# Kernel optimization log

Measured on AMD Instinct MI355X. Metric: run time of the kernel, lower is better.

## Reference

```python
import jax, jax.numpy as jnp
import numpy as np

B, N, F_IN, F_OUT = 8, 8192, 128, 128
EPS = 1e-12  # F.normalize default eps


def setup_inputs() -> dict:
    key = jax.random.key(0)
    k1, k2, k3, k4 = jax.random.split(key, 4)
    x = jax.random.normal(k1, (B, N, F_IN), dtype=jnp.float32)
    adj = jax.random.uniform(k2, (N, N), dtype=jnp.float32)
    weight = jax.random.normal(k3, (F_IN, F_OUT), dtype=jnp.float32) * 0.05
    bias = jax.random.normal(k4, (F_OUT,), dtype=jnp.float32) * 0.05
    return {"x": x, "adj": adj, "weight": weight, "bias": bias}


def reference(x, adj, weight, bias):
    # Aggregate: equivalent to torch.sparse.mm(adj, x^T.reshape(N, B*F)) then
    # un-reshape/transpose — i.e. y[b] = adj @ x[b] for every batch element.
    y = jnp.einsum('nm,bmf->bnf', adj, x)  # [B, N, F_in]
    y = y + x                               # add_self
    y = jnp.einsum('bnf,fo->bno', y, weight) + bias  # dense transform + bias
    # L2 normalize along feature dim (F.normalize, p=2, dim=2)
    norm = jnp.sqrt(jnp.sum(y * y, axis=2, keepdims=True))
    y = y / jnp.maximum(norm, EPS)
    return y
```

## Files before the change

### kernel.cpp

```cpp
#include <hip/hip_runtime.h>
#include <hip/hip_bf16.h>
#include <stdint.h>


typedef __bf16 bf16;
typedef __bf16 bf16x4 __attribute__((ext_vector_type(4)));
typedef __bf16 bf16x8 __attribute__((ext_vector_type(8)));
typedef float floatx4 __attribute__((ext_vector_type(4)));

#define B_ 8
#define N_ 8192
#define F_ 128

__device__ __forceinline__ void async_copy16(const void* g, void* l) {
  __builtin_amdgcn_global_load_lds(
      (const __attribute__((address_space(1))) uint32_t*)g,
      (__attribute__((address_space(3))) uint32_t*)l, 16, 0, 0);
}

__global__ __launch_bounds__(256, 2) void k0_xw_t(const float* __restrict__ x,
                                                  const float* __restrict__ w,
                                                  bf16* __restrict__ ut) {
  __shared__ bf16 As[128][128];
  __shared__ bf16 Wt[128][128];
  const int tid = threadIdx.x;
  const int lane = tid & 63;
  const int l15 = lane & 15;
  const int h = lane >> 4;
  const int wv = tid >> 6;
  const int wr = wv >> 1;
  const int wc = wv & 1;
  const int bm0 = blockIdx.x << 7;
  const int b = bm0 >> 13;
  const int m0 = bm0 & (N_ - 1);

#pragma unroll
  for (int c = 0; c < 64; ++c) {
    int lin = (c << 8) + tid;
    int f = lin >> 7, o = lin & 127;
    bf16 v = (bf16)w[(size_t)f * F_ + o];
    int phys = (f >> 3) ^ (o & 15);
    ((bf16*)Wt)[o * 128 + (phys << 3) + (f & 7)] = v;
  }

  {
    const int r = tid >> 1;
    const int colh = (tid & 1) << 6;
    const float* xr = x + (size_t)(bm0 + r) * F_ + colh;
#pragma unroll
    for (int q = 0; q < 8; ++q) {
      float4 f0 = *(const float4*)(xr + 8 * q);
      float4 f1 = *(const float4*)(xr + 8 * q + 4);
      bf16x8 pk;
      pk[0] = (bf16)f0.x; pk[1] = (bf16)f0.y; pk[2] = (bf16)f0.z; pk[3] = (bf16)f0.w;
      pk[4] = (bf16)f1.x; pk[5] = (bf16)f1.y; pk[6] = (bf16)f1.z; pk[7] = (bf16)f1.w;
      int c = ((tid & 1) << 3) + q;
      int phys = c ^ (r & 15);
      *(bf16x8*)&((bf16*)As)[r * 128 + (phys << 3)] = pk;
    }
  }
  __syncthreads();

  const bf16* pa[4][4];
  const bf16* pb[4][4];
#pragma unroll
  for (int i = 0; i < 4; ++i)
#pragma unroll
    for (int kk = 0; kk < 4; ++kk)
      pa[i][kk] = &As[64 * wr + 16 * i + l15][(((kk << 2) + h) ^ l15) << 3];
#pragma unroll
  for (int j = 0; j < 4; ++j)
#pragma unroll
    for (int kk = 0; kk < 4; ++kk)
      pb[j][kk] = &Wt[64 * wc + 16 * j + l15][(((kk << 2) + h) ^ l15) << 3];

  floatx4 acc[4][4] = {};
#pragma unroll
  for (int kk = 0; kk < 4; ++kk) {
    bf16x8 av[4], bv[4];
#pragma unroll
    for (int i = 0; i < 4; ++i) av[i] = *(const bf16x8*)pa[i][kk];
#pragma unroll
    for (int j = 0; j < 4; ++j) bv[j] = *(const bf16x8*)pb[j][kk];
#pragma unroll
    for (int i = 0; i < 4; ++i)
#pragma unroll
      for (int j = 0; j < 4; ++j)
        acc[i][j] = __builtin_amdgcn_mfma_f32_16x16x32_bf16(av[i], bv[j],
                                                            acc[i][j], 0, 0, 0);
  }

  bf16* utb = ut + (size_t)b * F_ * N_;
#pragma unroll
  for (int i = 0; i < 4; ++i)
#pragma unroll
    for (int j = 0; j < 4; ++j) {
      const int o = 64 * wc + 16 * j + l15;
      const int mrow = m0 + 64 * wr + 16 * i + (h << 2);
      bf16x4 pk;
#pragma unroll
      for (int r = 0; r < 4; ++r) pk[r] = (bf16)acc[i][j][r];
      *(bf16x4*)(utb + (size_t)o * N_ + mrow) = pk;
    }
}

__global__ __launch_bounds__(512, 4) void k1_graphconv(const float* __restrict__ adj,
                                                       const bf16* __restrict__ ut,
                                                       const float* __restrict__ bias,
                                                       float* __restrict__ out) {
  __shared__ bf16 As[128][64];
  __shared__ bf16 Bs[128][64];
  __shared__ float ss[2][128];
  const int tid = threadIdx.x;
  const int lane = tid & 63;
  const int wv = tid >> 6;
  const int wr = wv >> 1;
  const int wc = wv & 1;
  const int n0 = blockIdx.x << 7;
  const int b = blockIdx.y;
  const bf16* ub = ut + (size_t)b * F_ * N_;

  const int brow = tid >> 3;
  const int blc = (tid & 7) ^ (brow & 7);
  const bf16* gb0 = ub + (size_t)brow * N_ + (blc << 3);
  const bf16* gb1 = ub + (size_t)(brow + 64) * N_ + (blc << 3);
  bf16* lb0 = (bf16*)Bs + tid * 8;
  bf16* lb1 = (bf16*)Bs + (tid + 512) * 8;

  const int ar = tid >> 2;
  const int kc = (tid & 3) << 4;
  const float* gAb = adj + (size_t)(n0 + ar) * N_ + kc;
  const int pc0 = ((tid & 3) << 1) ^ (ar & 7);
  bf16* lA0 = (bf16*)As + ar * 64 + (pc0 << 3);
  bf16* lA1 = (bf16*)As + ar * 64 + ((pc0 ^ 1) << 3);

  const bf16* pa[2][2];
  const bf16* pb[4][2];
#pragma unroll
  for (int i = 0; i < 2; ++i)
#pragma unroll
    for (int kk = 0; kk < 2; ++kk)
      pa[i][kk] = &As[32 * wr + 16 * i + (lane & 15)]
                     [(((kk << 2) + (lane >> 4)) ^ (lane & 7)) << 3];
#pragma unroll
  for (int j = 0; j < 4; ++j)
#pragma unroll
    for (int kk = 0; kk < 2; ++kk)
      pb[j][kk] = &Bs[64 * wc + 16 * j + (lane & 15)]
                     [(((kk << 2) + (lane >> 4)) ^ (lane & 7)) << 3];

  floatx4 acc[2][4] = {};

  float4 pf[4];
#pragma unroll
  for (int q = 0; q < 4; ++q) pf[q] = *(const float4*)(gAb + 4 * q);

  for (int ks = 0; ks < 128; ++ks) {
    __syncthreads();
    async_copy16(gb0, lb0);
    async_copy16(gb1, lb1);
    gb0 += 64; gb1 += 64;
    bf16x8 lo, hi;
#pragma unroll
    for (int q = 0; q < 2; ++q) {
      float4 f = pf[q];
      lo[4 * q + 0] = (bf16)f.x; lo[4 * q + 1] = (bf16)f.y;
      lo[4 * q + 2] = (bf16)f.z; lo[4 * q + 3] = (bf16)f.w;
    }
#pragma unroll
    for (int q = 0; q < 2; ++q) {
      float4 f = pf[q + 2];
      hi[4 * q + 0] = (bf16)f.x; hi[4 * q + 1] = (bf16)f.y;
      hi[4 * q + 2] = (bf16)f.z; hi[4 * q + 3] = (bf16)f.w;
    }
    *(bf16x8*)lA0 = lo;
    *(bf16x8*)lA1 = hi;
    __syncthreads();
    const float* gn = gAb + ((size_t)((ks + 1) & 127) << 6);
#pragma unroll
    for (int q = 0; q < 4; ++q) pf[q] = *(const float4*)(gn + 4 * q);

#pragma unroll
    for (int kk = 0; kk < 2; ++kk) {
      bf16x8 av[2], bv[4];
#pragma unroll
      for (int i = 0; i < 2; ++i) av[i] = *(const bf16x8*)pa[i][kk];
#pragma unroll
      for (int j = 0; j < 4; ++j) bv[j] = *(const bf16x8*)pb[j][kk];
#pragma unroll
      for (int i = 0; i < 2; ++i)
#pragma unroll
        for (int j = 0; j < 4; ++j)
          acc[i][j] = __builtin_amdgcn_mfma_f32_16x16x32_bf16(av[i], bv[j],
                                                              acc[i][j], 0, 0, 0);
    }
  }

  float bo[4];
#pragma unroll
  for (int j = 0; j < 4; ++j) bo[j] = bias[64 * wc + 16 * j + (lane & 15)];

  float s[2][4];
#pragma unroll
  for (int i = 0; i < 2; ++i)
#pragma unroll
    for (int r = 0; r < 4; ++r) s[i][r] = 0.0f;
#pragma unroll
  for (int i = 0; i < 2; ++i)
#pragma unroll
    for (int j = 0; j < 4; ++j) {
      floatx4 t = acc[i][j];
      const int col = 64 * wc + 16 * j + (lane & 15);
#pragma unroll
      for (int r = 0; r < 4; ++r) {
        const int rowloc = 32 * wr + 16 * i + ((lane >> 4) << 2) + r;
        t[r] += bo[j] + (float)ub[(size_t)col * N_ + n0 + rowloc];
        s[i][r] += t[r] * t[r];
      }
      acc[i][j] = t;
    }
#pragma unroll
  for (int m = 1; m < 16; m <<= 1)
#pragma unroll
    for (int i = 0; i < 2; ++i)
#pragma unroll
      for (int r = 0; r < 4; ++r) s[i][r] += __shfl_xor(s[i][r], m, 16);

  if ((lane & 15) == 0) {
#pragma unroll
    for (int i = 0; i < 2; ++i)
#pragma unroll
      for (int r = 0; r < 4; ++r)
        ss[wc][32 * wr + 16 * i + ((lane >> 4) << 2) + r] = s[i][r];
  }
  __syncthreads();

  const size_t outbase = ((size_t)b * N_ + n0) * F_;
#pragma unroll
  for (int i = 0; i < 2; ++i)
#pragma unroll
    for (int r = 0; r < 4; ++r) {
      int rowloc = 32 * wr + 16 * i + ((lane >> 4) << 2) + r;
      float tot = ss[0][rowloc] + ss[1][rowloc];
      float inv = 1.0f / fmaxf(sqrtf(tot), 1e-12f);
      size_t ro = outbase + (size_t)rowloc * F_ + 64 * wc + (lane & 15);
#pragma unroll
      for (int j = 0; j < 4; ++j)
        out[ro + 16 * j] = acc[i][j][r] * inv;
    }
}

extern "C" void kernel_launch(void* const* d_in, const int* in_sizes, int n_in,
                              void* d_out, int out_size, void* d_ws, size_t ws_size,
                              hipStream_t stream) {
  (void)in_sizes; (void)n_in; (void)out_size; (void)ws_size;
  const float* x    = (const float*)d_in[0];
  const float* adj  = (const float*)d_in[1];
  const float* w    = (const float*)d_in[2];
  const float* bias = (const float*)d_in[3];
  float* out = (float*)d_out;
  bf16* ut = (bf16*)d_ws;

  k0_xw_t<<<dim3(512), dim3(256), 0, stream>>>(x, w, ut);
  k1_graphconv<<<dim3(64, 8), dim3(512), 0, stream>>>(adj, ut, bias, out);
}
```

Measured before the change: 543.3 us.

## Pretranspose weight once and restructure XW kernel to reuse graphconv pipeline

Adds a single-block kernel that converts the weight to bf16 and transposes it once, so each of the 512 XW blocks no longer converts and scatters the full 128x128 fp32 weight with scalar LDS stores. The XW kernel now uses 512 threads, smaller LDS tiles and the same async global-to-LDS K-loop as the main graphconv kernel, which raises occupancy. The cost is an extra kernel launch and a serial dependency. The XW stage is small next to the N×N adjacency GEMM, so the overall effect should be limited.

```diff
diff --git a/kernel.cpp b/kernel.cpp
--- a/kernel.cpp
+++ b/kernel.cpp
@@ -18,15 +18,41 @@
       (__attribute__((address_space(3))) uint32_t*)l, 16, 0, 0);
 }
 
-__global__ __launch_bounds__(256, 2) void k0_xw_t(const float* __restrict__ x,
-                                                  const float* __restrict__ w,
+__global__ __launch_bounds__(256) void k0w(const float* __restrict__ w,
+                                           bf16* __restrict__ wt) {
+  __shared__ bf16 T[128][129];
+  const int tid = threadIdx.x;
+#pragma unroll
+  for (int c = 0; c < 16; ++c) {
+    int lin = (c << 8) + tid;
+    int f = lin >> 5;
+    int g = lin & 31;
+    float4 v = *(const float4*)(w + (size_t)f * F_ + (g << 2));
+    T[f][(g << 2) + 0] = (bf16)v.x;
+    T[f][(g << 2) + 1] = (bf16)v.y;
+    T[f][(g << 2) + 2] = (bf16)v.z;
+    T[f][(g << 2) + 3] = (bf16)v.w;
+  }
+  __syncthreads();
+#pragma unroll
+  for (int c = 0; c < 16; ++c) {
+    int lin = (c << 8) + tid;
+    int o = lin >> 5;
+    int g = lin & 31;
+    bf16x4 pk;
+#pragma unroll
+    for (int q = 0; q < 4; ++q) pk[q] = T[(g << 2) + q][o];
+    *(bf16x4*)(wt + (size_t)o * F_ + (g << 2)) = pk;
+  }
+}
+
+__global__ __launch_bounds__(512, 4) void k0_xw_t(const float* __restrict__ x,
+                                                  const bf16* __restrict__ wt,
                                                   bf16* __restrict__ ut) {
-  __shared__ bf16 As[128][128];
-  __shared__ bf16 Wt[128][128];
+  __shared__ bf16 As[128][64];
+  __shared__ bf16 Bs[128][64];
   const int tid = threadIdx.x;
   const int lane = tid & 63;
-  const int l15 = lane & 15;
-  const int h = lane >> 4;
   const int wv = tid >> 6;
   const int wr = wv >> 1;
   const int wc = wv & 1;
@@ -34,69 +60,90 @@
   const int b = bm0 >> 13;
   const int m0 = bm0 & (N_ - 1);
 
-#pragma unroll
-  for (int c = 0; c < 64; ++c) {
-    int lin = (c << 8) + tid;
-    int f = lin >> 7, o = lin & 127;
-    bf16 v = (bf16)w[(size_t)f * F_ + o];
-    int phys = (f >> 3) ^ (o & 15);
-    ((bf16*)Wt)[o * 128 + (phys << 3) + (f & 7)] = v;
-  }
-
-  {
-    const int r = tid >> 1;
-    const int colh = (tid & 1) << 6;
-    const float* xr = x + (size_t)(bm0 + r) * F_ + colh;
-#pragma unroll
-    for (int q = 0; q < 8; ++q) {
-      float4 f0 = *(const float4*)(xr + 8 * q);
-      float4 f1 = *(const float4*)(xr + 8 * q + 4);
-      bf16x8 pk;
-      pk[0] = (bf16)f0.x; pk[1] = (bf16)f0.y; pk[2] = (bf16)f0.z; pk[3] = (bf16)f0.w;
-      pk[4] = (bf16)f1.x; pk[5] = (bf16)f1.y; pk[6] = (bf16)f1.z; pk[7] = (bf16)f1.w;
-      int c = ((tid & 1) << 3) + q;
-      int phys = c ^ (r & 15);
-      *(bf16x8*)&((bf16*)As)[r * 128 + (phys << 3)] = pk;
-    }
-  }
-  __syncthreads();
-
-  const bf16* pa[4][4];
-  const bf16* pb[4][4];
-#pragma unroll
-  for (int i = 0; i < 4; ++i)
-#pragma unroll
-    for (int kk = 0; kk < 4; ++kk)
-      pa[i][kk] = &As[64 * wr + 16 * i + l15][(((kk << 2) + h) ^ l15) << 3];
+  const int brow = tid >> 3;
+  const int blc = (tid & 7) ^ (brow & 7);
+  const bf16* gb0 = wt + (size_t)brow * F_ + (blc << 3);
+  const bf16* gb1 = wt + (size_t)(brow + 64) * F_ + (blc << 3);
+  bf16* lb0 = (bf16*)Bs + tid * 8;
+  bf16* lb1 = (bf16*)Bs + (tid + 512) * 8;
+
+  const int ar = tid >> 2;
+  const int kc = (tid & 3) << 4;
+  const float* gAb = x + (size_t)(bm0 + ar) * F_ + kc;
+  const int pc0 = ((tid & 3) << 1) ^ (ar & 7);
+  bf16* lA0 = (bf16*)As + ar * 64 + (pc0 << 3);
+  bf16* lA1 = (bf16*)As + ar * 64 + ((pc0 ^ 1) << 3);
+
+  const bf16* pa[2][2];
+  const bf16* pb[4][2];
+#pragma unroll
+  for (int i = 0; i < 2; ++i)
+#pragma unroll
+    for (int kk = 0; kk < 2; ++kk)
+      pa[i][kk] = &As[32 * wr + 16 * i + (lane & 15)]
+                     [(((kk << 2) + (lane >> 4)) ^ (lane & 7)) << 3];
 #pragma unroll
   for (int j = 0; j < 4; ++j)
 #pragma unroll
-    for (int kk = 0; kk < 4; ++kk)
-      pb[j][kk] = &Wt[64 * wc + 16 * j + l15][(((kk << 2) + h) ^ l15) << 3];
-
-  floatx4 acc[4][4] = {};
-#pragma unroll
-  for (int kk = 0; kk < 4; ++kk) {
-    bf16x8 av[4], bv[4];
-#pragma unroll
-    for (int i = 0; i < 4; ++i) av[i] = *(const bf16x8*)pa[i][kk];
-#pragma unroll
-    for (int j = 0; j < 4; ++j) bv[j] = *(const bf16x8*)pb[j][kk];
-#pragma unroll
-    for (int i = 0; i < 4; ++i)
-#pragma unroll
-      for (int j = 0; j < 4; ++j)
-        acc[i][j] = __builtin_amdgcn_mfma_f32_16x16x32_bf16(av[i], bv[j],
-                                                            acc[i][j], 0, 0, 0);
+    for (int kk = 0; kk < 2; ++kk)
+      pb[j][kk] = &Bs[64 * wc + 16 * j + (lane & 15)]
+                     [(((kk << 2) + (lane >> 4)) ^ (lane & 7)) << 3];
+
+  floatx4 acc[2][4] = {};
+
+  float4 pf[4];
+#pragma unroll
+  for (int q = 0; q < 4; ++q) pf[q] = *(const float4*)(gAb + 4 * q);
+
+#pragma unroll
+  for (int ks = 0; ks < 2; ++ks) {
+    __syncthreads();
+    async_copy16(gb0, lb0);
+    async_copy16(gb1, lb1);
+    gb0 += 64; gb1 += 64;
+    bf16x8 lo, hi;
+#pragma unroll
+    for (int q = 0; q < 2; ++q) {
+      float4 f = pf[q];
+      lo[4 * q + 0] = (bf16)f.x; lo[4 * q + 1] = (bf16)f.y;
+      lo[4 * q + 2] = (bf16)f.z; lo[4 * q + 3] = (bf16)f.w;
+    }
+#pragma unroll
+    for (int q = 0; q < 2; ++q) {
+      float4 f = pf[q + 2];
+      hi[4 * q + 0] = (bf16)f.x; hi[4 * q + 1] = (bf16)f.y;
+      hi[4 * q + 2] = (bf16)f.z; hi[4 * q + 3] = (bf16)f.w;
+    }
+    *(bf16x8*)lA0 = lo;
+    *(bf16x8*)lA1 = hi;
+    __syncthreads();
+    const float* gn = gAb + (((ks + 1) & 1) << 6);
+#pragma unroll
+    for (int q = 0; q < 4; ++q) pf[q] = *(const float4*)(gn + 4 * q);
+
+#pragma unroll
+    for (int kk = 0; kk < 2; ++kk) {
+      bf16x8 av[2], bv[4];
+#pragma unroll
+      for (int i = 0; i < 2; ++i) av[i] = *(const bf16x8*)pa[i][kk];
+#pragma unroll
+      for (int j = 0; j < 4; ++j) bv[j] = *(const bf16x8*)pb[j][kk];
+#pragma unroll
+      for (int i = 0; i < 2; ++i)
+#pragma unroll
+        for (int j = 0; j < 4; ++j)
+          acc[i][j] = __builtin_amdgcn_mfma_f32_16x16x32_bf16(av[i], bv[j],
+                                                              acc[i][j], 0, 0, 0);
+    }
   }
 
   bf16* utb = ut + (size_t)b * F_ * N_;
 #pragma unroll
-  for (int i = 0; i < 4; ++i)
+  for (int i = 0; i < 2; ++i)
 #pragma unroll
     for (int j = 0; j < 4; ++j) {
-      const int o = 64 * wc + 16 * j + l15;
-      const int mrow = m0 + 64 * wr + 16 * i + (h << 2);
+      const int o = 64 * wc + 16 * j + (lane & 15);
+      const int mrow = m0 + 32 * wr + 16 * i + ((lane >> 4) << 2);
       bf16x4 pk;
 #pragma unroll
       for (int r = 0; r < 4; ++r) pk[r] = (bf16)acc[i][j][r];
@@ -260,7 +307,9 @@
   const float* bias = (const float*)d_in[3];
   float* out = (float*)d_out;
   bf16* ut = (bf16*)d_ws;
-
-  k0_xw_t<<<dim3(512), dim3(256), 0, stream>>>(x, w, ut);
+  bf16* wt = ut + (size_t)B_ * F_ * N_;
+
+  k0w<<<dim3(1), dim3(256), 0, stream>>>(w, wt);
+  k0_xw_t<<<dim3(512), dim3(512), 0, stream>>>(x, wt, ut);
   k1_graphconv<<<dim3(64, 8), dim3(512), 0, stream>>>(adj, ut, bias, out);
 }
```

Result: no change. 545.2 us (+0.3%).
